# Optimization experiments

Hardware: AMD Instinct MI355X
Metric: run time of the kernel (lower is better)

## Reference

```python
import jax, jax.numpy as jnp
import numpy as np

USER_NUM = 100000
ITEM_NUM = 50000
E = 128   # embedding_size
A = 64    # attention_size
M = 8     # memory_size
B = 4096  # batch
NF = 50   # friends per user


def _l2norm(x, axis):
    # torch F.normalize(p=2): x / max(||x||, eps)
    n = jnp.sqrt(jnp.sum(x * x, axis=axis, keepdims=True))
    return x / jnp.maximum(n, 1e-12)


def setup_inputs() -> dict:
    key = jax.random.key(0)
    ks = jax.random.split(key, 9)
    u = lambda k, shape: jax.random.uniform(k, shape, jnp.float32, -0.1, 0.1)
    return {
        "input_u": jax.random.randint(ks[0], (B,), 0, USER_NUM),
        "input_i": jax.random.randint(ks[1], (B,), 0, ITEM_NUM),
        "input_uf": jax.random.randint(ks[2], (B, NF), 0, USER_NUM + 1),
        "uidW": u(ks[3], (USER_NUM + 1, E)),
        "iidW": u(ks[4], (ITEM_NUM, E)),
        "i_bias": jnp.zeros((ITEM_NUM,), jnp.float32),
        "Key": u(ks[5], (E, M)),
        "Mem": jnp.ones((M, E), jnp.float32),
        "WA": u(ks[6], (E, A)),
        "BA": jnp.zeros((A,), jnp.float32),
        "U_omega": u(ks[7], (A, 1)),
    }


def reference(input_u, input_i, input_uf, uidW, iidW, i_bias, Key, Mem, WA, BA, U_omega):
    user_num = uidW.shape[0] - 1  # padding id
    uid = uidW[input_u]                      # [B, E]
    iid = iidW[input_i]                      # [B, E]
    i_b = i_bias[input_i]                    # [B]
    fe = uidW[input_uf]                      # [B, F, E] friend embeddings
    fn = (input_uf != user_num).astype(uid.dtype)  # [B, F] valid-friend mask

    fe = fn[:, :, None] * fe
    uid_n = _l2norm(uid, axis=1)
    fe_n = _l2norm(fe, axis=2)
    cross = uid_n[:, None, :] * fe_n                     # [B, F, E]
    att_key = jnp.einsum('bfe,em->bfm', cross, Key)      # [B, F, M]
    att_mem = jax.nn.softmax(att_key, axis=0)            # softmax over batch (faithful to dim=0)
    att_mem = fn[:, :, None] * att_mem
    f1 = jnp.einsum('bfm,me->bfe', att_mem, Mem)         # [B, F, E]
    f2 = f1 * fe
    h = jax.nn.relu(jnp.einsum('bfe,ea->bfa', f2, WA) + BA)
    j = jnp.exp(jnp.einsum('bfa,ao->bfo', h, U_omega))   # [B, F, 1]
    j = fn[:, :, None] * j
    w = j / (jnp.sum(j, axis=1, keepdims=True) + 1e-8)
    friend = jnp.sum(w * f2, axis=1)                     # [B, E] (dropout p=0 -> identity)
    user = uid + friend
    score = jnp.sum(user * iid, axis=1) + i_b            # [B]
    return score
```

## Files before the change

kernel.cpp:

```cpp
#include <hip/hip_runtime.h>

#define EDIM 128
#define MDIM 8
#define ADIM 64
#define NFR  50
#define NCOL (NFR * MDIM)

typedef __attribute__((ext_vector_type(8))) short short8;
typedef __attribute__((ext_vector_type(4))) float f32x4;

__device__ __forceinline__ float waveReduceSum(float v) {
    #pragma unroll
    for (int s = 32; s >= 1; s >>= 1) v += __shfl_xor(v, s, 64);
    return v;
}
__device__ __forceinline__ short f2bf(float x) {
    unsigned u = __float_as_uint(x);
    u += 0x7FFFu + ((u >> 16) & 1u);
    return (short)(u >> 16);
}

__global__ __launch_bounds__(256)
void k0_prep(const float* __restrict__ WA, const float* __restrict__ Mem,
             const float* __restrict__ Key,
             short* __restrict__ WATf, short* __restrict__ MemTf,
             short* __restrict__ KeyTf)
{
    int t = blockIdx.x * 256 + threadIdx.x;
    int lane = t & 63, c = lane & 15, g = (lane >> 4) & 3;
    short8 v = {0, 0, 0, 0, 0, 0, 0, 0};
    if (t < 1024) {
        int frag = t >> 6, Ma = frag >> 2, Kt = frag & 3;
        int a = Ma * 16 + c;
        #pragma unroll
        for (int j = 0; j < 8; ++j) {
            int e = Kt * 32 + g * 8 + j;
            v[j] = f2bf(WA[(size_t)e * ADIM + a]);
        }
        *(short8*)(WATf + (size_t)t * 8) = v;
    } else if (t < 1536) {
        int i = t - 1024, Mt = i >> 6;
        int e = Mt * 16 + c;
        #pragma unroll
        for (int j = 0; j < 8; ++j) {
            int k = g * 8 + j;
            v[j] = (k < MDIM) ? f2bf(Mem[(size_t)k * EDIM + e]) : (short)0;
        }
        *(short8*)(MemTf + (size_t)i * 8) = v;
    } else if (t < 1792) {
        int i = t - 1536, Kt = i >> 6;
        #pragma unroll
        for (int j = 0; j < 8; ++j) {
            int e = Kt * 32 + g * 8 + j;
            v[j] = (c < MDIM) ? f2bf(Key[(size_t)e * MDIM + c]) : (short)0;
        }
        *(short8*)(KeyTf + (size_t)i * 8) = v;
    }
}

__global__ __launch_bounds__(256, 4)
void k1_attkey(const int* __restrict__ input_u, const int* __restrict__ input_uf,
               const float* __restrict__ uidW, const short* __restrict__ KeyTf,
               float* __restrict__ att_key, int user_num)
{
    const int b = blockIdx.x, t = threadIdx.x, w = t >> 6, l = t & 63;
    const int c = l & 15, g = l >> 4;
    __shared__ float uidn[EDIM];
    __shared__ float redW[4];
    __shared__ int ufL[64];

    if (t < 64) ufL[t] = (t < NFR) ? input_uf[(size_t)b * NFR + t] : user_num;
    const int u = input_u[b];
    float x = (t < EDIM) ? uidW[(size_t)u * EDIM + t] : 0.f;
    float ss = waveReduceSum(x * x);
    if (l == 0) redW[w] = ss;
    __syncthreads();
    float uinv = 1.0f / fmaxf(sqrtf(redW[0] + redW[1] + redW[2] + redW[3]), 1e-12f);
    if (t < EDIM) uidn[t] = x * uinv;
    __syncthreads();

    const int f = w * 16 + c;
    const int fid = ufL[f];
    const float fn = (f < NFR && fid != user_num) ? 1.0f : 0.0f;
    const float* fp = uidW + (size_t)fid * EDIM;

    float4 fe[4][2];
    #pragma unroll
    for (int Kt = 0; Kt < 4; ++Kt) {
        fe[Kt][0] = *(const float4*)(fp + Kt * 32 + g * 8);
        fe[Kt][1] = *(const float4*)(fp + Kt * 32 + g * 8 + 4);
    }
    float fss = 0.f;
    #pragma unroll
    for (int Kt = 0; Kt < 4; ++Kt)
        #pragma unroll
        for (int h = 0; h < 2; ++h) {
            float4 q = fe[Kt][h];
            fss += q.x * q.x + q.y * q.y + q.z * q.z + q.w * q.w;
        }
    fss += __shfl_xor(fss, 16, 64);
    fss += __shfl_xor(fss, 32, 64);
    const float inv2 = fn / fmaxf(sqrtf(fss), 1e-12f);

    f32x4 acc = {0.f, 0.f, 0.f, 0.f};
    #pragma unroll
    for (int Kt = 0; Kt < 4; ++Kt) {
        float4 un0 = *(const float4*)&uidn[Kt * 32 + g * 8];
        float4 un1 = *(const float4*)&uidn[Kt * 32 + g * 8 + 4];
        short8 bf;
        bf[0] = f2bf(un0.x * fe[Kt][0].x * inv2);
        bf[1] = f2bf(un0.y * fe[Kt][0].y * inv2);
        bf[2] = f2bf(un0.z * fe[Kt][0].z * inv2);
        bf[3] = f2bf(un0.w * fe[Kt][0].w * inv2);
        bf[4] = f2bf(un1.x * fe[Kt][1].x * inv2);
        bf[5] = f2bf(un1.y * fe[Kt][1].y * inv2);
        bf[6] = f2bf(un1.z * fe[Kt][1].z * inv2);
        bf[7] = f2bf(un1.w * fe[Kt][1].w * inv2);
        short8 af = *(const short8*)(KeyTf + (size_t)(Kt * 64 + l) * 8);
        acc = __builtin_amdgcn_mfma_f32_16x16x32_bf16(af, bf, acc, 0, 0, 0);
    }
    if (f < NFR && g < 2) {
        float4 st = {acc[0], acc[1], acc[2], acc[3]};
        *(float4*)&att_key[(size_t)b * NCOL + f * MDIM + g * 4] = st;
    }
}

__global__ __launch_bounds__(256)
void k2a_stats(const float* __restrict__ ak,
               float* __restrict__ Pm, float* __restrict__ Ps, int B)
{
    const int cg = blockIdx.x;
    const int rc = blockIdx.y;
    const int t = threadIdx.x;
    const int c = t & 15, r = t >> 4;
    const int col = cg * 16 + c;
    const int base = rc * (B >> 4);

    float x[16];
    #pragma unroll
    for (int k = 0; k < 16; ++k)
        x[k] = ak[(size_t)(base + k * 16 + r) * NCOL + col];
    float m = x[0];
    #pragma unroll
    for (int k = 1; k < 16; ++k) m = fmaxf(m, x[k]);
    float s = 0.f;
    #pragma unroll
    for (int k = 0; k < 16; ++k) s += __expf(x[k] - m);

    __shared__ float mL[16][17], sL[16][17];
    mL[r][c] = m; sL[r][c] = s;
    __syncthreads();
    if (t < 16) {
        float M = mL[0][t];
        #pragma unroll
        for (int rr = 1; rr < 16; ++rr) M = fmaxf(M, mL[rr][t]);
        float S = 0.f;
        #pragma unroll
        for (int rr = 0; rr < 16; ++rr) S += sL[rr][t] * __expf(mL[rr][t] - M);
        Pm[rc * NCOL + cg * 16 + t] = M;
        Ps[rc * NCOL + cg * 16 + t] = S;
    }
}

__global__ __launch_bounds__(256, 4)
void k3_final(const int* __restrict__ input_u, const int* __restrict__ input_i,
              const int* __restrict__ input_uf, const float* __restrict__ uidW,
              const float* __restrict__ iidW, const float* __restrict__ i_bias,
              const short* __restrict__ WATf, const short* __restrict__ MemTf,
              const float* __restrict__ BA, const float* __restrict__ U_omega,
              const float* __restrict__ att_key,
              const float* __restrict__ Pm, const float* __restrict__ Ps,
              float* __restrict__ out, int user_num)
{
    const int b = blockIdx.x, t = threadIdx.x, w = t >> 6, l = t & 63;
    const int c = l & 15, g = l >> 4;
    __shared__ short WATs[16 * 64 * 8];
    __shared__ short f2s[4][4 * 64 * 8];
    __shared__ float amL[512];
    __shared__ float uidL[EDIM], iidL[EDIM];
    __shared__ float baL[ADIM], uoL[ADIM];
    __shared__ int ufL[64];
    __shared__ float sjW[4], syW[4];

    if (t < 64) ufL[t] = (t < NFR) ? input_uf[(size_t)b * NFR + t] : user_num;
    __syncthreads();

    const int u = input_u[b];
    const int ii = input_i[b];
    if (t < EDIM) {
        uidL[t] = uidW[(size_t)u * EDIM + t];
        iidL[t] = iidW[(size_t)ii * EDIM + t];
    }
    if (t < ADIM) { baL[t] = BA[t]; uoL[t] = U_omega[t]; }

    {
        const uint4* src = (const uint4*)WATf;
        uint4* dst = (uint4*)WATs;
        #pragma unroll
        for (int i = 0; i < 4; ++i) dst[t + 256 * i] = src[t + 256 * i];
    }

    const int f = w * 16 + c;
    const int fid = ufL[f];
    const float fn = (f < NFR && fid != user_num) ? 1.0f : 0.0f;
    float4 fe4[8];
    {
        const float* fp = uidW + (size_t)fid * EDIM;
        #pragma unroll
        for (int Mt = 0; Mt < 8; ++Mt)
            fe4[Mt] = *(const float4*)(fp + Mt * 16 + g * 4);
    }

    for (int i = t; i < 512; i += 256) {
        float amv = 0.f;
        if (i < NCOL) {
            float M = -3.4e38f;
            #pragma unroll
            for (int rc = 0; rc < 16; ++rc) M = fmaxf(M, Pm[rc * NCOL + i]);
            float S = 0.f;
            #pragma unroll
            for (int rc = 0; rc < 16; ++rc)
                S += Ps[rc * NCOL + i] * __expf(Pm[rc * NCOL + i] - M);
            float ak = att_key[(size_t)b * NCOL + i];
            if (ufL[i >> 3] != user_num) amv = __expf(ak - M) / S;
        }
        amL[i] = amv;
    }
    __syncthreads();

    short8 amf = {0, 0, 0, 0, 0, 0, 0, 0};
    if (g == 0) {
        float4 a0 = *(const float4*)&amL[f * 8];
        float4 a1 = *(const float4*)&amL[f * 8 + 4];
        amf[0] = f2bf(a0.x); amf[1] = f2bf(a0.y);
        amf[2] = f2bf(a0.z); amf[3] = f2bf(a0.w);
        amf[4] = f2bf(a1.x); amf[5] = f2bf(a1.y);
        amf[6] = f2bf(a1.z); amf[7] = f2bf(a1.w);
    }

    f32x4 C1[8];
    #pragma unroll
    for (int Mt = 0; Mt < 8; ++Mt) {
        short8 af = *(const short8*)(MemTf + (size_t)(Mt * 64 + l) * 8);
        f32x4 z = {0.f, 0.f, 0.f, 0.f};
        C1[Mt] = __builtin_amdgcn_mfma_f32_16x16x32_bf16(af, amf, z, 0, 0, 0);
    }

    #pragma unroll
    for (int Mt = 0; Mt < 8; ++Mt) {
        float q0 = C1[Mt][0] * fe4[Mt].x * fn;
        float q1 = C1[Mt][1] * fe4[Mt].y * fn;
        float q2 = C1[Mt][2] * fe4[Mt].z * fn;
        float q3 = C1[Mt][3] * fe4[Mt].w * fn;
        unsigned d0 = ((unsigned)(unsigned short)f2bf(q0)) |
                      (((unsigned)(unsigned short)f2bf(q1)) << 16);
        unsigned d1 = ((unsigned)(unsigned short)f2bf(q2)) |
                      (((unsigned)(unsigned short)f2bf(q3)) << 16);
        int lane2 = ((Mt & 1) * 2 + (g >> 1)) * 16 + c;
        int off = ((Mt >> 1) * 64 + lane2) * 8 + (g & 1) * 4;
        uint2 dd = {d0, d1};
        *(uint2*)&f2s[w][off] = dd;
    }

    f32x4 C2[4], C3 = {0.f, 0.f, 0.f, 0.f};
    #pragma unroll
    for (int Ma = 0; Ma < 4; ++Ma) C2[Ma] = (f32x4){0.f, 0.f, 0.f, 0.f};
    #pragma unroll
    for (int Kt = 0; Kt < 4; ++Kt) {
        short8 bf = *(const short8*)&f2s[w][(Kt * 64 + l) * 8];
        #pragma unroll
        for (int Ma = 0; Ma < 4; ++Ma) {
            short8 af = *(const short8*)&WATs[((Ma * 4 + Kt) * 64 + l) * 8];
            C2[Ma] = __builtin_amdgcn_mfma_f32_16x16x32_bf16(af, bf, C2[Ma], 0, 0, 0);
        }
        short8 itf = {0, 0, 0, 0, 0, 0, 0, 0};
        if (c == 0) {
            float4 i0 = *(const float4*)&iidL[Kt * 32 + g * 8];
            float4 i1 = *(const float4*)&iidL[Kt * 32 + g * 8 + 4];
            itf[0] = f2bf(i0.x); itf[1] = f2bf(i0.y);
            itf[2] = f2bf(i0.z); itf[3] = f2bf(i0.w);
            itf[4] = f2bf(i1.x); itf[5] = f2bf(i1.y);
            itf[6] = f2bf(i1.z); itf[7] = f2bf(i1.w);
        }
        C3 = __builtin_amdgcn_mfma_f32_16x16x32_bf16(itf, bf, C3, 0, 0, 0);
    }

    float psum = 0.f;
    #pragma unroll
    for (int Ma = 0; Ma < 4; ++Ma) {
        float4 ba4 = *(const float4*)&baL[Ma * 16 + g * 4];
        float4 uo4 = *(const float4*)&uoL[Ma * 16 + g * 4];
        psum += fmaxf(C2[Ma][0] + ba4.x, 0.f) * uo4.x;
        psum += fmaxf(C2[Ma][1] + ba4.y, 0.f) * uo4.y;
        psum += fmaxf(C2[Ma][2] + ba4.z, 0.f) * uo4.z;
        psum += fmaxf(C2[Ma][3] + ba4.w, 0.f) * uo4.w;
    }
    psum += __shfl_xor(psum, 16, 64);
    psum += __shfl_xor(psum, 32, 64);
    const float jv = (fn > 0.f) ? __expf(psum) : 0.f;
    const float jy = jv * C3[0];
    float sj = waveReduceSum((g == 0) ? jv : 0.f);
    float sy = waveReduceSum(jy);
    if (l == 0) { sjW[w] = sj; syW[w] = sy; }
    __syncthreads();

    if (w == 0) {
        float s = uidL[l] * iidL[l] + uidL[l + 64] * iidL[l + 64];
        s = waveReduceSum(s);
        if (l == 0) {
            float Sj = sjW[0] + sjW[1] + sjW[2] + sjW[3] + 1e-8f;
            float Sy = syW[0] + syW[1] + syW[2] + syW[3];
            out[b] = s + Sy / Sj + i_bias[ii];
        }
    }
}

extern "C" void kernel_launch(void* const* d_in, const int* in_sizes, int n_in,
                              void* d_out, int out_size, void* d_ws, size_t ws_size,
                              hipStream_t stream)
{
    const int*   input_u  = (const int*)d_in[0];
    const int*   input_i  = (const int*)d_in[1];
    const int*   input_uf = (const int*)d_in[2];
    const float* uidW     = (const float*)d_in[3];
    const float* iidW     = (const float*)d_in[4];
    const float* i_bias   = (const float*)d_in[5];
    const float* Key      = (const float*)d_in[6];
    const float* Mem      = (const float*)d_in[7];
    const float* WA       = (const float*)d_in[8];
    const float* BA       = (const float*)d_in[9];
    const float* U_om     = (const float*)d_in[10];

    const int B = in_sizes[0];
    const int user_num = in_sizes[3] / EDIM - 1;

    float* att = (float*)d_ws;
    float* Pm  = att + (size_t)B * NCOL;
    float* Ps  = Pm + 16 * NCOL;
    short* WATf  = (short*)(Ps + 16 * NCOL);
    short* MemTf = WATf + 16 * 64 * 8;
    short* KeyTf = MemTf + 8 * 64 * 8;

    k0_prep<<<7, 256, 0, stream>>>(WA, Mem, Key, WATf, MemTf, KeyTf);
    k1_attkey<<<B, 256, 0, stream>>>(input_u, input_uf, uidW, KeyTf, att, user_num);
    k2a_stats<<<dim3(25, 16), 256, 0, stream>>>(att, Pm, Ps, B);
    k3_final<<<B, 256, 0, stream>>>(input_u, input_i, input_uf, uidW, iidW, i_bias,
                                    WATf, MemTf, BA, U_om, att, Pm, Ps,
                                    (float*)d_out, user_num);
}
```

Baseline: 175.9 us.

## Replace max-stabilized batch softmax with unshifted exp sums and reciprocal

k1 now stores exp(att_key) directly, and the column statistics drop the running-max two-pass scheme in favour of a plain partial-sum kernel plus a single-block merge that produces reciprocal sums. k3 then computes each attention weight as one multiply instead of recombining 16 partial max/sum pairs per column in every block. k3 also reads the WA bf16 tiles straight from global memory instead of staging them in LDS, and both big kernels raise their occupancy hint from 4 to 6. Skipping the max shift relies on the attention logits staying small enough that exp cannot overflow, which holds for normalized inputs but is less robust in general. It also adds a serial single-block merge launch.

```diff
diff --git a/kernel.cpp b/kernel.cpp
--- a/kernel.cpp
+++ b/kernel.cpp
@@ -5,6 +5,7 @@
 #define ADIM 64
 #define NFR  50
 #define NCOL (NFR * MDIM)
+#define NPART 256
 
 typedef __attribute__((ext_vector_type(8))) short short8;
 typedef __attribute__((ext_vector_type(4))) float f32x4;
@@ -58,10 +59,10 @@
     }
 }
 
-__global__ __launch_bounds__(256, 4)
+__global__ __launch_bounds__(256, 6)
 void k1_attkey(const int* __restrict__ input_u, const int* __restrict__ input_uf,
                const float* __restrict__ uidW, const short* __restrict__ KeyTf,
-               float* __restrict__ att_key, int user_num)
+               float* __restrict__ eatt, int user_num)
 {
     const int b = blockIdx.x, t = threadIdx.x, w = t >> 6, l = t & 63;
     const int c = l & 15, g = l >> 4;
@@ -120,61 +121,64 @@
         acc = __builtin_amdgcn_mfma_f32_16x16x32_bf16(af, bf, acc, 0, 0, 0);
     }
     if (f < NFR && g < 2) {
-        float4 st = {acc[0], acc[1], acc[2], acc[3]};
-        *(float4*)&att_key[(size_t)b * NCOL + f * MDIM + g * 4] = st;
+        float4 st = {__expf(acc[0]), __expf(acc[1]), __expf(acc[2]), __expf(acc[3])};
+        *(float4*)&eatt[(size_t)b * NCOL + f * MDIM + g * 4] = st;
     }
 }
 
 __global__ __launch_bounds__(256)
-void k2a_stats(const float* __restrict__ ak,
-               float* __restrict__ Pm, float* __restrict__ Ps, int B)
-{
-    const int cg = blockIdx.x;
-    const int rc = blockIdx.y;
-    const int t = threadIdx.x;
-    const int c = t & 15, r = t >> 4;
-    const int col = cg * 16 + c;
-    const int base = rc * (B >> 4);
-
-    float x[16];
-    #pragma unroll
-    for (int k = 0; k < 16; ++k)
-        x[k] = ak[(size_t)(base + k * 16 + r) * NCOL + col];
-    float m = x[0];
-    #pragma unroll
-    for (int k = 1; k < 16; ++k) m = fmaxf(m, x[k]);
-    float s = 0.f;
-    #pragma unroll
-    for (int k = 0; k < 16; ++k) s += __expf(x[k] - m);
-
-    __shared__ float mL[16][17], sL[16][17];
-    mL[r][c] = m; sL[r][c] = s;
-    __syncthreads();
-    if (t < 16) {
-        float M = mL[0][t];
-        #pragma unroll
-        for (int rr = 1; rr < 16; ++rr) M = fmaxf(M, mL[rr][t]);
-        float S = 0.f;
-        #pragma unroll
-        for (int rr = 0; rr < 16; ++rr) S += sL[rr][t] * __expf(mL[rr][t] - M);
-        Pm[rc * NCOL + cg * 16 + t] = M;
-        Ps[rc * NCOL + cg * 16 + t] = S;
-    }
-}
-
-__global__ __launch_bounds__(256, 4)
+void k2a_sum(const float* __restrict__ eatt, float* __restrict__ partial, int B)
+{
+    const int blk = blockIdx.x, t = threadIdx.x, w = t >> 6, l = t & 63;
+    __shared__ float colS[4][NCOL];
+    const int rowsPerBlk = B / NPART;
+    const int rowsPerWave = rowsPerBlk >> 2;
+    const int r0 = blk * rowsPerBlk + w * rowsPerWave;
+
+    float4 a1 = {0.f, 0.f, 0.f, 0.f}, a2 = {0.f, 0.f, 0.f, 0.f};
+    for (int it = 0; it < rowsPerWave; ++it) {
+        const float* row = eatt + (size_t)(r0 + it) * NCOL;
+        float4 v1 = *(const float4*)(row + 4 * l);
+        a1.x += v1.x; a1.y += v1.y; a1.z += v1.z; a1.w += v1.w;
+        if (l < 36) {
+            float4 v2 = *(const float4*)(row + 256 + 4 * l);
+            a2.x += v2.x; a2.y += v2.y; a2.z += v2.z; a2.w += v2.w;
+        }
+    }
+    *(float4*)&colS[w][4 * l] = a1;
+    if (l < 36) *(float4*)&colS[w][256 + 4 * l] = a2;
+    __syncthreads();
+    if (t < 256)
+        partial[(size_t)blk * NCOL + t] =
+            colS[0][t] + colS[1][t] + colS[2][t] + colS[3][t];
+    if (t < 144) {
+        int c2 = 256 + t;
+        partial[(size_t)blk * NCOL + c2] =
+            colS[0][c2] + colS[1][c2] + colS[2][c2] + colS[3][c2];
+    }
+}
+
+__global__ __launch_bounds__(512)
+void k2b_merge(const float* __restrict__ partial, float* __restrict__ ise)
+{
+    int c = threadIdx.x;
+    if (c >= NCOL) return;
+    float S = 0.f;
+    for (int b = 0; b < NPART; ++b) S += partial[(size_t)b * NCOL + c];
+    ise[c] = 1.0f / S;
+}
+
+__global__ __launch_bounds__(256, 6)
 void k3_final(const int* __restrict__ input_u, const int* __restrict__ input_i,
               const int* __restrict__ input_uf, const float* __restrict__ uidW,
               const float* __restrict__ iidW, const float* __restrict__ i_bias,
               const short* __restrict__ WATf, const short* __restrict__ MemTf,
               const float* __restrict__ BA, const float* __restrict__ U_omega,
-              const float* __restrict__ att_key,
-              const float* __restrict__ Pm, const float* __restrict__ Ps,
+              const float* __restrict__ eatt, const float* __restrict__ ise,
               float* __restrict__ out, int user_num)
 {
     const int b = blockIdx.x, t = threadIdx.x, w = t >> 6, l = t & 63;
     const int c = l & 15, g = l >> 4;
-    __shared__ short WATs[16 * 64 * 8];
     __shared__ short f2s[4][4 * 64 * 8];
     __shared__ float amL[512];
     __shared__ float uidL[EDIM], iidL[EDIM];
@@ -193,13 +197,6 @@
     }
     if (t < ADIM) { baL[t] = BA[t]; uoL[t] = U_omega[t]; }
 
-    {
-        const uint4* src = (const uint4*)WATf;
-        uint4* dst = (uint4*)WATs;
-        #pragma unroll
-        for (int i = 0; i < 4; ++i) dst[t + 256 * i] = src[t + 256 * i];
-    }
-
     const int f = w * 16 + c;
     const int fid = ufL[f];
     const float fn = (f < NFR && fid != user_num) ? 1.0f : 0.0f;
@@ -213,17 +210,8 @@
 
     for (int i = t; i < 512; i += 256) {
         float amv = 0.f;
-        if (i < NCOL) {
-            float M = -3.4e38f;
-            #pragma unroll
-            for (int rc = 0; rc < 16; ++rc) M = fmaxf(M, Pm[rc * NCOL + i]);
-            float S = 0.f;
-            #pragma unroll
-            for (int rc = 0; rc < 16; ++rc)
-                S += Ps[rc * NCOL + i] * __expf(Pm[rc * NCOL + i] - M);
-            float ak = att_key[(size_t)b * NCOL + i];
-            if (ufL[i >> 3] != user_num) amv = __expf(ak - M) / S;
-        }
+        if (i < NCOL && ufL[i >> 3] != user_num)
+            amv = eatt[(size_t)b * NCOL + i] * ise[i];
         amL[i] = amv;
     }
     __syncthreads();
@@ -270,7 +258,7 @@
         short8 bf = *(const short8*)&f2s[w][(Kt * 64 + l) * 8];
         #pragma unroll
         for (int Ma = 0; Ma < 4; ++Ma) {
-            short8 af = *(const short8*)&WATs[((Ma * 4 + Kt) * 64 + l) * 8];
+            short8 af = *(const short8*)(WATf + (size_t)((Ma * 4 + Kt) * 64 + l) * 8);
             C2[Ma] = __builtin_amdgcn_mfma_f32_16x16x32_bf16(af, bf, C2[Ma], 0, 0, 0);
         }
         short8 itf = {0, 0, 0, 0, 0, 0, 0, 0};
@@ -334,17 +322,18 @@
     const int B = in_sizes[0];
     const int user_num = in_sizes[3] / EDIM - 1;
 
-    float* att = (float*)d_ws;
-    float* Pm  = att + (size_t)B * NCOL;
-    float* Ps  = Pm + 16 * NCOL;
-    short* WATf  = (short*)(Ps + 16 * NCOL);
+    float* eatt = (float*)d_ws;
+    float* partial = eatt + (size_t)B * NCOL;
+    float* ise = partial + (size_t)NPART * NCOL;
+    short* WATf  = (short*)(ise + NCOL);
     short* MemTf = WATf + 16 * 64 * 8;
     short* KeyTf = MemTf + 8 * 64 * 8;
 
     k0_prep<<<7, 256, 0, stream>>>(WA, Mem, Key, WATf, MemTf, KeyTf);
-    k1_attkey<<<B, 256, 0, stream>>>(input_u, input_uf, uidW, KeyTf, att, user_num);
-    k2a_stats<<<dim3(25, 16), 256, 0, stream>>>(att, Pm, Ps, B);
+    k1_attkey<<<B, 256, 0, stream>>>(input_u, input_uf, uidW, KeyTf, eatt, user_num);
+    k2a_sum<<<NPART, 256, 0, stream>>>(eatt, partial, B);
+    k2b_merge<<<1, 512, 0, stream>>>(partial, ise);
     k3_final<<<B, 256, 0, stream>>>(input_u, input_i, input_uf, uidW, iidW, i_bias,
-                                    WATf, MemTf, BA, U_om, att, Pm, Ps,
+                                    WATf, MemTf, BA, U_om, eatt, ise,
                                     (float*)d_out, user_num);
 }
```

Result: slower. 181.0 us (+2.9%).
